# Performance work log

Hardware: AMD Instinct MI355X
Metric: run time of the kernel (lower is better)

Reference implementation:

```python
import jax, jax.numpy as jnp
import numpy as np

B, S, D = 2, 2048, 1024
H, DK, DV = 16, 64, 64
DF = 4096
EPS = 1e-5


def _layer_norm(x, g, b):
    mu = jnp.mean(x, axis=-1, keepdims=True)
    var = jnp.mean((x - mu) ** 2, axis=-1, keepdims=True)
    return (x - mu) * jax.lax.rsqrt(var + EPS) * g + b


def setup_inputs() -> dict:
    key = jax.random.key(0)
    ks = jax.random.split(key, 12)
    s = lambda fan_in: 1.0 / np.sqrt(fan_in)
    return {
        "enc_input": jax.random.normal(ks[0], (B, S, D), dtype=jnp.float32),
        "wq": jax.random.uniform(ks[1], (D, H * DK), jnp.float32, -s(D), s(D)),
        "wk": jax.random.uniform(ks[2], (D, H * DK), jnp.float32, -s(D), s(D)),
        "wv": jax.random.uniform(ks[3], (D, H * DV), jnp.float32, -s(D), s(D)),
        "wo": jax.random.uniform(ks[4], (H * DV, D), jnp.float32, -s(H * DV), s(H * DV)),
        "w1": jax.random.uniform(ks[5], (D, DF), jnp.float32, -s(D), s(D)),
        "b1": jax.random.uniform(ks[6], (DF,), jnp.float32, -s(D), s(D)),
        "w2": jax.random.uniform(ks[7], (DF, D), jnp.float32, -s(DF), s(DF)),
        "b2": jax.random.uniform(ks[8], (D,), jnp.float32, -s(DF), s(DF)),
        "ln1_g": jnp.ones((D,), jnp.float32),
        "ln1_b": jnp.zeros((D,), jnp.float32),
        "ln2_g": jnp.ones((D,), jnp.float32),
        "ln2_b": jnp.zeros((D,), jnp.float32),
    }


def reference(enc_input, wq, wk, wv, wo, w1, b1, w2, b2, ln1_g, ln1_b, ln2_g, ln2_b):
    x = enc_input
    # QKV projections -> [B, H, S, d]
    q = (x @ wq).reshape(B, S, H, DK).transpose(0, 2, 1, 3)
    k = (x @ wk).reshape(B, S, H, DK).transpose(0, 2, 1, 3)
    v = (x @ wv).reshape(B, S, H, DV).transpose(0, 2, 1, 3)
    # scaled dot-product attention (scale = 1/sqrt(d_k), dropout is identity at eval)
    score = jnp.einsum("bhqd,bhkd->bhqk", q, k) / jnp.sqrt(jnp.float32(DK))
    attn = jax.nn.softmax(score, axis=-1)
    ctx = jnp.einsum("bhqk,bhkd->bhqd", attn, v)
    ctx = ctx.transpose(0, 2, 1, 3).reshape(B, S, H * DV)
    atn_out = ctx @ wo
    # Add & Norm 1
    h = _layer_norm(x + atn_out, ln1_g, ln1_b)
    # FFN
    ffn = jax.nn.relu(h @ w1 + b1) @ w2 + b2
    # Add & Norm 2
    return _layer_norm(h + ffn, ln2_g, ln2_b)
```

## Files before the change

### kernel.cpp

```cpp
#include <hip/hip_runtime.h>
#include <hip/hip_bf16.h>

typedef __bf16 bf16;
typedef __bf16 bf16x4 __attribute__((ext_vector_type(4)));
typedef __bf16 bf16x8 __attribute__((ext_vector_type(8)));
typedef float  f32x4  __attribute__((ext_vector_type(4)));

#define KB 2
#define KS 2048
#define KD 1024
#define KH 16
#define KM (KB*KS)
#define KQKVN 3072
#define KDF 4096

__device__ __forceinline__ f32x4 mfma16(bf16x8 a, bf16x8 b, f32x4 c) {
  return __builtin_amdgcn_mfma_f32_16x16x32_bf16(a, b, c, 0, 0, 0);
}

__device__ __forceinline__ float exp2_hw(float x) {
  float r;
  asm("v_exp_f32 %0, %1" : "=v"(r) : "v"(x));
  return r;
}

__device__ __forceinline__ void g2l16(const bf16* g, bf16* l) {
  __builtin_amdgcn_global_load_lds(
      (const __attribute__((address_space(1))) unsigned int*)g,
      (__attribute__((address_space(3))) unsigned int*)l, 16, 0, 0);
}

__global__ __launch_bounds__(256) void cvt_bf16_kernel(const float* __restrict__ in,
                                                       bf16* __restrict__ out, int n) {
  int i = (blockIdx.x * 256 + threadIdx.x) * 4;
  if (i >= n) return;
  f32x4 v = *reinterpret_cast<const f32x4*>(in + i);
  bf16x4 o;
  o[0] = (bf16)v[0]; o[1] = (bf16)v[1]; o[2] = (bf16)v[2]; o[3] = (bf16)v[3];
  *reinterpret_cast<bf16x4*>(out + i) = o;
}

struct WT4 { const float* src[4]; bf16* dst[4]; };

__global__ __launch_bounds__(256) void wtrans4_kernel(WT4 jobs) {
  __shared__ float tile[32][33];
  const float* W = jobs.src[blockIdx.z];
  bf16* WT = jobs.dst[blockIdx.z];
  const int n0 = blockIdx.x * 32, k0 = blockIdx.y * 32;
  const int tx = threadIdx.x & 31, ty = threadIdx.x >> 5;
#pragma unroll
  for (int j = ty; j < 32; j += 8) tile[j][tx] = W[(size_t)(k0 + j) * 1024 + n0 + tx];
  __syncthreads();
#pragma unroll
  for (int j = ty; j < 32; j += 8)
    WT[(size_t)(n0 + j) * 1024 + k0 + tx] = (bf16)tile[tx][j];
}

__global__ __launch_bounds__(256) void wtrans_big_kernel(const float* __restrict__ w1,
                                                         bf16* __restrict__ w1T,
                                                         const float* __restrict__ w2,
                                                         bf16* __restrict__ w2T) {
  __shared__ float tile[32][33];
  const float* W; bf16* WT; int K, N, n0, k0;
  if (blockIdx.z == 0) {
    W = w1; WT = w1T; K = 1024; N = 4096;
    n0 = blockIdx.x * 32; k0 = blockIdx.y * 32;
  } else {
    W = w2; WT = w2T; K = 4096; N = 1024;
    n0 = blockIdx.y * 32; k0 = blockIdx.x * 32;
  }
  const int tx = threadIdx.x & 31, ty = threadIdx.x >> 5;
#pragma unroll
  for (int j = ty; j < 32; j += 8) tile[j][tx] = W[(size_t)(k0 + j) * N + n0 + tx];
  __syncthreads();
#pragma unroll
  for (int j = ty; j < 32; j += 8) WT[(size_t)(n0 + j) * K + k0 + tx] = (bf16)tile[tx][j];
}

struct P4 { bf16* p[4]; };

template <typename OUT_T, bool RELU, bool HAS_BIAS, bool SPLITK, bool QKVPACK>
__global__ __launch_bounds__(512, 2) void gemm8p(const bf16* __restrict__ A,
                                                 const bf16* __restrict__ BT,
                                                 OUT_T* __restrict__ C, P4 pr,
                                                 const float* __restrict__ bias,
                                                 int M, int N, int K, int Kslice) {
  extern __shared__ __align__(16) bf16 sm[];
  const int tid = threadIdx.x, lane = tid & 63, w = tid >> 6;
  const int wr = w >> 2, wc = w & 3;
  const int gx = gridDim.x;
  const int nwg = gx * gridDim.y;
  int flat = blockIdx.y * gx + blockIdx.x;
  flat = (flat & 7) * (nwg >> 3) + (flat >> 3);
  const int bn = (flat % gx) * 256;
  const int bm = (flat / gx) * 256;
  const int z = blockIdx.z;
  const int NT = (SPLITK ? Kslice : K) >> 6;
  const int lr = lane & 15, hi = lane >> 4;
  const int sqrow = tid >> 3;
  const int sslot = tid & 7;
  const bf16* Abase = A + (size_t)bm * K + (SPLITK ? z * Kslice : 0);
  const bf16* Bbase = BT + (size_t)bn * K + (SPLITK ? z * Kslice : 0);
  auto stageQ = [&](int t, int p) {
    const int row = p * 64 + sqrow;
    const int col = (sslot ^ (row & 7)) * 8;
    bf16* dst = sm + (size_t)(t & 1) * 32768 + p * 4096 + w * 512;
    g2l16(Abase + (size_t)row * K + t * 64 + col, dst);
    g2l16(Bbase + (size_t)row * K + t * 64 + col, dst + 16384);
  };
  f32x4 acc[8][4] = {};
  stageQ(0, 0); stageQ(0, 1); stageQ(0, 2); stageQ(0, 3);
  for (int t = 0; t < NT; t++) {
    const char* sa = (const char*)(sm + (size_t)(t & 1) * 32768);
    const char* sb = sa + 32768;
    if (t + 1 < NT) {
      stageQ(t + 1, 0);
      stageQ(t + 1, 1);
      asm volatile("s_waitcnt vmcnt(4)" ::: "memory");
    } else {
      asm volatile("s_waitcnt vmcnt(0)" ::: "memory");
    }
    __builtin_amdgcn_sched_barrier(0);
    __builtin_amdgcn_s_barrier();
    __builtin_amdgcn_sched_barrier(0);
    if (t + 1 < NT) { stageQ(t + 1, 2); stageQ(t + 1, 3); }
    bf16x8 af[4], bfr[4];
#pragma unroll
    for (int mfp = 0; mfp < 4; mfp++) {
      const int row = wr * 128 + mfp * 16 + lr;
      af[mfp] = *(const bf16x8*)(sa + row * 128 + ((hi ^ (row & 7)) * 16));
    }
#pragma unroll
    for (int nf = 0; nf < 4; nf++) {
      const int row = wc * 64 + nf * 16 + lr;
      bfr[nf] = *(const bf16x8*)(sb + row * 128 + ((hi ^ (row & 7)) * 16));
    }
    __builtin_amdgcn_s_setprio(1);
#pragma unroll
    for (int mfp = 0; mfp < 4; mfp++)
#pragma unroll
      for (int nf = 0; nf < 4; nf++)
        acc[mfp][nf] = mfma16(af[mfp], bfr[nf], acc[mfp][nf]);
    __builtin_amdgcn_s_setprio(0);
#pragma unroll
    for (int mfp = 0; mfp < 4; mfp++) {
      const int row = wr * 128 + 64 + mfp * 16 + lr;
      af[mfp] = *(const bf16x8*)(sa + row * 128 + ((hi ^ (row & 7)) * 16));
    }
    __builtin_amdgcn_s_setprio(1);
#pragma unroll
    for (int mfp = 0; mfp < 4; mfp++)
#pragma unroll
      for (int nf = 0; nf < 4; nf++)
        acc[4 + mfp][nf] = mfma16(af[mfp], bfr[nf], acc[4 + mfp][nf]);
    __builtin_amdgcn_s_setprio(0);
#pragma unroll
    for (int mfp = 0; mfp < 4; mfp++) {
      const int row = wr * 128 + mfp * 16 + lr;
      af[mfp] = *(const bf16x8*)(sa + row * 128 + (((4 + hi) ^ (row & 7)) * 16));
    }
#pragma unroll
    for (int nf = 0; nf < 4; nf++) {
      const int row = wc * 64 + nf * 16 + lr;
      bfr[nf] = *(const bf16x8*)(sb + row * 128 + (((4 + hi) ^ (row & 7)) * 16));
    }
    __builtin_amdgcn_s_setprio(1);
#pragma unroll
    for (int mfp = 0; mfp < 4; mfp++)
#pragma unroll
      for (int nf = 0; nf < 4; nf++)
        acc[mfp][nf] = mfma16(af[mfp], bfr[nf], acc[mfp][nf]);
    __builtin_amdgcn_s_setprio(0);
#pragma unroll
    for (int mfp = 0; mfp < 4; mfp++) {
      const int row = wr * 128 + 64 + mfp * 16 + lr;
      af[mfp] = *(const bf16x8*)(sa + row * 128 + (((4 + hi) ^ (row & 7)) * 16));
    }
    __builtin_amdgcn_s_setprio(1);
#pragma unroll
    for (int mfp = 0; mfp < 4; mfp++)
#pragma unroll
      for (int nf = 0; nf < 4; nf++)
        acc[4 + mfp][nf] = mfma16(af[mfp], bfr[nf], acc[4 + mfp][nf]);
    __builtin_amdgcn_s_setprio(0);
    __builtin_amdgcn_sched_barrier(0);
    __builtin_amdgcn_s_barrier();
    __builtin_amdgcn_sched_barrier(0);
  }
  const int rg = hi * 4, cl = lr;
  if (QKVPACK && (bn >> 10) == 1) {
    bf16* kp_ = pr.p[0];
    const int b_ = bm >> 11;
    const int sb_ = (bm & 2047) + wr * 128;
#pragma unroll
    for (int mf = 0; mf < 8; mf++)
#pragma unroll
      for (int nf = 0; nf < 4; nf++) {
        const int col_loc = (bn & 1023) + wc * 64 + nf * 16 + cl;
        const int hh = col_loc >> 6, dd = col_loc & 63;
        bf16* base = kp_ + (size_t)(b_ * 16 + hh) * (KS * 64) + dd;
#pragma unroll
        for (int i = 0; i < 4; i++)
          base[(size_t)(sb_ + mf * 16 + rg + i) * 64] = (bf16)acc[mf][nf][i];
      }
  } else if (QKVPACK && (bn >> 10) == 2) {
    bf16* vt_ = pr.p[1];
    const int b_ = bm >> 11;
    const int sb_ = (bm & 2047) + wr * 128;
    const int pib = ((hi & 2) << 3) | ((hi & 1) << 3);
#pragma unroll
    for (int mf = 0; mf < 8; mf++) {
      const int s_hi = sb_ + (mf >> 2) * 64;
      const int pibase = pib | ((mf & 2) << 4) | ((mf & 1) << 2);
#pragma unroll
      for (int nf = 0; nf < 4; nf++) {
        const int col_loc = (bn & 1023) + wc * 64 + nf * 16 + cl;
        const int hh = col_loc >> 6, dd = col_loc & 63;
        bf16x4 o;
#pragma unroll
        for (int i = 0; i < 4; i++) o[i] = (bf16)acc[mf][nf][i];
        *(bf16x4*)(vt_ + (size_t)(b_ * 16 + hh) * (64 * KS) +
                   (size_t)dd * KS + s_hi + pibase) = o;
      }
    }
  } else if (SPLITK) {
    bf16* P = pr.p[z];
#pragma unroll
    for (int mf = 0; mf < 8; mf++)
#pragma unroll
      for (int nf = 0; nf < 4; nf++) {
        const int col = bn + wc * 64 + nf * 16 + cl;
#pragma unroll
        for (int i = 0; i < 4; i++) {
          const int row = bm + wr * 128 + mf * 16 + rg + i;
          P[(size_t)row * N + col] = (bf16)acc[mf][nf][i];
        }
      }
  } else {
#pragma unroll
    for (int mf = 0; mf < 8; mf++)
#pragma unroll
      for (int nf = 0; nf < 4; nf++) {
        const int col = bn + wc * 64 + nf * 16 + cl;
        float bv = 0.f;
        if (HAS_BIAS) bv = bias[col];
#pragma unroll
        for (int i = 0; i < 4; i++) {
          const int row = bm + wr * 128 + mf * 16 + rg + i;
          float v = acc[mf][nf][i] + bv;
          if (RELU) v = fmaxf(v, 0.f);
          C[(size_t)row * N + col] = (OUT_T)v;
        }
      }
  }
}

template <typename OUT_T, bool RELU, bool HAS_BIAS, int BN>
__global__ __launch_bounds__(256) void gemm_bt(const bf16* __restrict__ A,
                                               const bf16* __restrict__ BT,
                                               OUT_T* __restrict__ C,
                                               const float* __restrict__ bias,
                                               int M, int N, int K) {
  constexpr int NF = BN / 32;
  __shared__ __align__(16) bf16 sa[2][128 * 32];
  __shared__ __align__(16) bf16 sb[2][BN * 32];
  const int t = threadIdx.x, lane = t & 63, w = t >> 6;
  const int gx = gridDim.x;
  const int nwg = gx * gridDim.y;
  int flat = blockIdx.y * gx + blockIdx.x;
  if ((nwg & 7) == 0) flat = (flat & 7) * (nwg >> 3) + (flat >> 3);
  const int bn = (flat % gx) * BN;
  const int bm = (flat / gx) * 128;
  const int wr = w >> 1, wc = w & 1;
  const int wcol = wc * (BN / 2);
  const int lr = lane & 15, lk = (lane >> 4) * 8;
  const int srow = w * 16 + (lane >> 2);
  const int scol = (lane & 3) * 8;
  f32x4 acc[4][NF] = {};
  const int NT = K >> 5;
  auto stage = [&](int kt, int buf) {
#pragma unroll
    for (int i = 0; i < 2; i++)
      g2l16(A + (size_t)(bm + i * 64 + srow) * K + kt * 32 + scol,
            &sa[buf][(i * 64 + w * 16) * 32]);
#pragma unroll
    for (int i = 0; i < BN / 64; i++)
      g2l16(BT + (size_t)(bn + i * 64 + srow) * K + kt * 32 + scol,
            &sb[buf][(i * 64 + w * 16) * 32]);
  };
  stage(0, 0);
  int cur = 0;
  for (int kt = 0; kt < NT; kt++) {
    __syncthreads();
    if (kt + 1 < NT) stage(kt + 1, cur ^ 1);
    bf16x8 af[4], bfr[NF];
#pragma unroll
    for (int m = 0; m < 4; m++)
      af[m] = *(const bf16x8*)&sa[cur][(wr * 64 + m * 16 + lr) * 32 + lk];
#pragma unroll
    for (int n = 0; n < NF; n++)
      bfr[n] = *(const bf16x8*)&sb[cur][(wcol + n * 16 + lr) * 32 + lk];
#pragma unroll
    for (int m = 0; m < 4; m++)
#pragma unroll
      for (int n = 0; n < NF; n++)
        acc[m][n] = mfma16(af[m], bfr[n], acc[m][n]);
    cur ^= 1;
  }
  const int rg = (lane >> 4) * 4, cl = lane & 15;
#pragma unroll
  for (int m = 0; m < 4; m++)
#pragma unroll
    for (int n = 0; n < NF; n++) {
      const int col = bn + wcol + n * 16 + cl;
      float bv = 0.f;
      if (HAS_BIAS) bv = bias[col];
#pragma unroll
      for (int i = 0; i < 4; i++) {
        const int row = bm + wr * 64 + m * 16 + rg + i;
        float v = acc[m][n][i] + bv;
        if (RELU) v = fmaxf(v, 0.f);
        C[(size_t)row * N + col] = (OUT_T)v;
      }
    }
}

__global__ __launch_bounds__(256) void attn_kernel(const bf16* __restrict__ qkv,
                                                   const bf16* __restrict__ kp,
                                                   const bf16* __restrict__ vt,
                                                   bf16* __restrict__ ctx) {
  __shared__ __align__(16) bf16 ksm[2][64 * 64];
  __shared__ __align__(16) bf16 vsm[2][64 * 64];
  const int t = threadIdx.x, lane = t & 63, w = t >> 6;
  const int flat = blockIdx.y * 32 + blockIdx.x;
  const int xcd = flat & 7, jj = flat >> 3;
  const int bh = xcd + 8 * (jj >> 5);
  const int qb = jj & 31;
  const int b = bh >> 4, h = bh & 15;
  const int qbase = qb * 64 + w * 16;
  const int lr = lane & 15, hi = lane >> 4;
  const int lk = hi * 8, rg = hi * 4, cl = lr;

  bf16x8 aq[2];
#pragma unroll
  for (int kk = 0; kk < 2; kk++) {
    bf16x8 v = *reinterpret_cast<const bf16x8*>(
        &qkv[(size_t)(b * KS + qbase + lr) * KQKVN + h * 64 + kk * 32 + lk]);
#pragma unroll
    for (int e = 0; e < 8; e++) v[e] = (bf16)((float)v[e] * 0.18033688f);
    aq[kk] = v;
  }
  bf16x8 ones;
#pragma unroll
  for (int j = 0; j < 8; j++) ones[j] = (bf16)1.0f;

  const bf16* kpb = kp + (size_t)bh * KS * 64;
  const bf16* vtb = vt + (size_t)bh * 64 * KS;

  auto stageKV = [&](int tt) {
    const int kt0 = tt * 64;
    bf16* kd = &ksm[tt & 1][0];
    bf16* vd = &vsm[tt & 1][0];
#pragma unroll
    for (int i = 0; i < 2; i++) {
      const int q = i * 4096 + w * 1024 + (lane << 4);
      const int row = q >> 7;
      const int slot = ((q >> 4) & 7) ^ (row & 7);
      g2l16(kpb + (size_t)(kt0 + row) * 64 + slot * 8, kd + ((i * 4096 + w * 1024) >> 1));
      g2l16(vtb + (size_t)row * KS + kt0 + slot * 8,   vd + ((i * 4096 + w * 1024) >> 1));
    }
  };

  f32x4 accd[4] = {};
  f32x4 lsumv = {};

  stageKV(0); stageKV(1);
  const int NT = KS / 64;
  for (int tt = 0; tt < NT; tt++) {
    if (tt + 1 < NT) asm volatile("s_waitcnt vmcnt(4)" ::: "memory");
    else             asm volatile("s_waitcnt vmcnt(0)" ::: "memory");
    __builtin_amdgcn_sched_barrier(0);
    __builtin_amdgcn_s_barrier();
    __builtin_amdgcn_sched_barrier(0);
    const char* kb = (const char*)&ksm[tt & 1][0];
    const char* vb = (const char*)&vsm[tt & 1][0];
    bf16x8 bk[4][2];
#pragma unroll
    for (int n = 0; n < 4; n++)
#pragma unroll
      for (int kk = 0; kk < 2; kk++) {
        const int row = n * 16 + lr;
        bk[n][kk] = *(const bf16x8*)(kb + row * 128 +
                                     ((kk * 64 + hi * 16) ^ ((row & 7) << 4)));
      }
    f32x4 sc[4] = {};
    __builtin_amdgcn_s_setprio(1);
#pragma unroll
    for (int n = 0; n < 4; n++)
#pragma unroll
      for (int kk = 0; kk < 2; kk++)
        sc[n] = mfma16(bk[n][kk], aq[kk], sc[n]);
    __builtin_amdgcn_s_setprio(0);
    bf16x8 pa[2];
    {
      float p[4][4];
#pragma unroll
      for (int n = 0; n < 4; n++)
#pragma unroll
        for (int i = 0; i < 4; i++)
          p[n][i] = exp2_hw(sc[n][i]);
#pragma unroll
      for (int kk = 0; kk < 2; kk++) {
        bf16x8 v;
#pragma unroll
        for (int j = 0; j < 8; j++) v[j] = (bf16)p[kk * 2 + (j >> 2)][j & 3];
        pa[kk] = v;
      }
    }
    bf16x8 bv[4][2];
#pragma unroll
    for (int dt = 0; dt < 4; dt++)
#pragma unroll
      for (int kk = 0; kk < 2; kk++) {
        const int row = dt * 16 + lr;
        bv[dt][kk] = *(const bf16x8*)(vb + row * 128 +
                                      ((kk * 64 + hi * 16) ^ ((row & 7) << 4)));
      }
    __builtin_amdgcn_s_setprio(1);
#pragma unroll
    for (int dt = 0; dt < 4; dt++)
#pragma unroll
      for (int kk = 0; kk < 2; kk++)
        accd[dt] = mfma16(pa[kk], bv[dt][kk], accd[dt]);
    lsumv = mfma16(pa[0], ones, lsumv);
    lsumv = mfma16(pa[1], ones, lsumv);
    __builtin_amdgcn_s_setprio(0);
    __builtin_amdgcn_sched_barrier(0);
    __builtin_amdgcn_s_barrier();
    __builtin_amdgcn_sched_barrier(0);
    if (tt + 2 < NT) stageKV(tt + 2);
  }
#pragma unroll
  for (int dt = 0; dt < 4; dt++)
#pragma unroll
    for (int i = 0; i < 4; i++)
      ctx[(size_t)(b * KS + qbase + rg + i) * KD + h * 64 + dt * 16 + cl] =
          (bf16)(accd[dt][i] / lsumv[i]);
}

template <bool ABF, bool BBF, bool OBF>
__global__ __launch_bounds__(256) void ln_kernel(const void* __restrict__ aptr,
                                                 const void* __restrict__ bptr,
                                                 const float* __restrict__ g,
                                                 const float* __restrict__ bet,
                                                 void* __restrict__ outp) {
  const int row = blockIdx.x;
  const int t = threadIdx.x;
  const int lane = t & 63, wid = t >> 6;
  float v[4];
  {
    float a[4], bb[4];
    if (ABF) {
      bf16x4 av = *reinterpret_cast<const bf16x4*>(
          (const bf16*)aptr + (size_t)row * KD + t * 4);
#pragma unroll
      for (int j = 0; j < 4; j++) a[j] = (float)av[j];
    } else {
      f32x4 av = *reinterpret_cast<const f32x4*>(
          (const float*)aptr + (size_t)row * KD + t * 4);
#pragma unroll
      for (int j = 0; j < 4; j++) a[j] = av[j];
    }
    if (BBF) {
      bf16x4 bv = *reinterpret_cast<const bf16x4*>(
          (const bf16*)bptr + (size_t)row * KD + t * 4);
#pragma unroll
      for (int j = 0; j < 4; j++) bb[j] = (float)bv[j];
    } else {
      f32x4 bv = *reinterpret_cast<const f32x4*>(
          (const float*)bptr + (size_t)row * KD + t * 4);
#pragma unroll
      for (int j = 0; j < 4; j++) bb[j] = bv[j];
    }
#pragma unroll
    for (int j = 0; j < 4; j++) v[j] = a[j] + bb[j];
  }
  float s = 0.f, s2 = 0.f;
#pragma unroll
  for (int j = 0; j < 4; j++) { s += v[j]; s2 += v[j] * v[j]; }
#pragma unroll
  for (int off = 32; off; off >>= 1) {
    s += __shfl_xor(s, off, 64);
    s2 += __shfl_xor(s2, off, 64);
  }
  __shared__ float red[8];
  if (lane == 0) { red[wid] = s; red[wid + 4] = s2; }
  __syncthreads();
  s = red[0] + red[1] + red[2] + red[3];
  s2 = red[4] + red[5] + red[6] + red[7];
  const float mu = s * (1.f / KD);
  const float var = s2 * (1.f / KD) - mu * mu;
  const float rs = rsqrtf(var + 1e-5f);
  if (OBF) {
    bf16x4 o;
#pragma unroll
    for (int j = 0; j < 4; j++)
      o[j] = (bf16)((v[j] - mu) * rs * g[t * 4 + j] + bet[t * 4 + j]);
    *reinterpret_cast<bf16x4*>((bf16*)outp + (size_t)row * KD + t * 4) = o;
  } else {
    f32x4 o;
#pragma unroll
    for (int j = 0; j < 4; j++)
      o[j] = (v[j] - mu) * rs * g[t * 4 + j] + bet[t * 4 + j];
    *reinterpret_cast<f32x4*>((float*)outp + (size_t)row * KD + t * 4) = o;
  }
}

__global__ __launch_bounds__(256) void ln2_fused_kernel(const bf16* __restrict__ hh,
                                                        const bf16* __restrict__ p0,
                                                        const bf16* __restrict__ p1,
                                                        const bf16* __restrict__ p2,
                                                        const bf16* __restrict__ p3,
                                                        const float* __restrict__ b2,
                                                        const float* __restrict__ g,
                                                        const float* __restrict__ bet,
                                                        float* __restrict__ outp) {
  const int row = blockIdx.x;
  const int t = threadIdx.x;
  const int lane = t & 63, wid = t >> 6;
  const size_t base = (size_t)row * KD + t * 4;
  bf16x4 hv = *(const bf16x4*)(hh + base);
  bf16x4 a0 = *(const bf16x4*)(p0 + base);
  bf16x4 a1 = *(const bf16x4*)(p1 + base);
  bf16x4 a2 = *(const bf16x4*)(p2 + base);
  bf16x4 a3 = *(const bf16x4*)(p3 + base);
  f32x4 bv = *(const f32x4*)(b2 + t * 4);
  float v[4];
#pragma unroll
  for (int j = 0; j < 4; j++)
    v[j] = (float)hv[j] + (float)a0[j] + (float)a1[j] + (float)a2[j] + (float)a3[j] + bv[j];
  float s = 0.f, s2 = 0.f;
#pragma unroll
  for (int j = 0; j < 4; j++) { s += v[j]; s2 += v[j] * v[j]; }
#pragma unroll
  for (int off = 32; off; off >>= 1) {
    s += __shfl_xor(s, off, 64);
    s2 += __shfl_xor(s2, off, 64);
  }
  __shared__ float red[8];
  if (lane == 0) { red[wid] = s; red[wid + 4] = s2; }
  __syncthreads();
  s = red[0] + red[1] + red[2] + red[3];
  s2 = red[4] + red[5] + red[6] + red[7];
  const float mu = s * (1.f / KD);
  const float var = s2 * (1.f / KD) - mu * mu;
  const float rs = rsqrtf(var + 1e-5f);
  f32x4 o;
#pragma unroll
  for (int j = 0; j < 4; j++)
    o[j] = (v[j] - mu) * rs * g[t * 4 + j] + bet[t * 4 + j];
  *reinterpret_cast<f32x4*>(outp + base) = o;
}

extern "C" void kernel_launch(void* const* d_in, const int* in_sizes, int n_in,
                              void* d_out, int out_size, void* d_ws, size_t ws_size,
                              hipStream_t stream) {
  const float* x     = (const float*)d_in[0];
  const float* wq    = (const float*)d_in[1];
  const float* wk    = (const float*)d_in[2];
  const float* wv    = (const float*)d_in[3];
  const float* wo    = (const float*)d_in[4];
  const float* w1    = (const float*)d_in[5];
  const float* b1    = (const float*)d_in[6];
  const float* w2    = (const float*)d_in[7];
  const float* b2    = (const float*)d_in[8];
  const float* ln1g  = (const float*)d_in[9];
  const float* ln1b  = (const float*)d_in[10];
  const float* ln2g  = (const float*)d_in[11];
  const float* ln2b  = (const float*)d_in[12];
  float* out = (float*)d_out;

  char* ws = (char*)d_ws;
  bf16*  x_bf   = (bf16*)(ws + 0);
  bf16*  wqkvT  = (bf16*)(ws + 8388608);
  bf16*  woT    = (bf16*)(ws + 14680064);
  bf16*  w1T    = (bf16*)(ws + 16777216);
  bf16*  w2T    = (bf16*)(ws + 25165824);
  bf16*  qkv    = (bf16*)(ws + 33554432);
  bf16*  kp     = (bf16*)(ws + 58720256);
  bf16*  vt     = (bf16*)(ws + 67108864);
  bf16*  ctx    = (bf16*)(ws + 75497472);
  bf16*  proj_bf= (bf16*)(ws + 83886080);
  bf16*  h_bf   = (bf16*)(ws + 8388608);
  bf16*  ffn1   = qkv;
  P4 pk;
  pk.p[0] = kp; pk.p[1] = vt; pk.p[2] = nullptr; pk.p[3] = nullptr;
  P4 pr;
  pr.p[0] = (bf16*)(ws + 0);
  pr.p[1] = (bf16*)(ws + 16777216);
  pr.p[2] = (bf16*)(ws + 67108864);
  pr.p[3] = (bf16*)(ws + 75497472);
  P4 pzero = {};

  cvt_bf16_kernel<<<dim3(KM * KD / 1024), 256, 0, stream>>>(x, x_bf, KM * KD);
  WT4 jobs;
  jobs.src[0] = wq; jobs.src[1] = wk; jobs.src[2] = wv; jobs.src[3] = wo;
  jobs.dst[0] = wqkvT;
  jobs.dst[1] = wqkvT + 1024 * 1024;
  jobs.dst[2] = wqkvT + 2048 * 1024;
  jobs.dst[3] = woT;
  wtrans4_kernel<<<dim3(32, 32, 4), 256, 0, stream>>>(jobs);
  wtrans_big_kernel<<<dim3(128, 32, 2), 256, 0, stream>>>(w1, w1T, w2, w2T);

  gemm8p<bf16, false, false, false, true>
      <<<dim3(KQKVN / 256, KM / 256, 1), 512, 131072, stream>>>(
      x_bf, wqkvT, qkv, pk, nullptr, KM, KQKVN, KD, KD);

  attn_kernel<<<dim3(KS / 64, KB * KH), 256, 0, stream>>>(qkv, kp, vt, ctx);

  gemm_bt<bf16, false, false, 64><<<dim3(KD / 64, KM / 128), 256, 0, stream>>>(
      ctx, woT, proj_bf, nullptr, KM, KD, KD);

  ln_kernel<true, true, true><<<dim3(KM), 256, 0, stream>>>(
      x_bf, proj_bf, ln1g, ln1b, h_bf);

  gemm8p<bf16, true, true, false, false>
      <<<dim3(KDF / 256, KM / 256, 1), 512, 131072, stream>>>(
      h_bf, w1T, ffn1, pzero, b1, KM, KDF, KD, KD);

  gemm8p<bf16, false, false, true, false>
      <<<dim3(KD / 256, KM / 256, 4), 512, 131072, stream>>>(
      ffn1, w2T, (bf16*)nullptr, pr, nullptr, KM, KD, KDF, KDF / 4);

  ln2_fused_kernel<<<dim3(KM), 256, 0, stream>>>(
      h_bf, pr.p[0], pr.p[1], pr.p[2], pr.p[3], b2, ln2g, ln2b, out);
}
```

Measured before the change: 221.6 us.

## Split attention over two KV halves with 32 queries per warp, add combine kernel

Each attention block now covers 128 queries (two 16-row query tiles per warp) but only half of the key/value sequence, so each staged K/V tile is reused across twice as many queries. The block writes unnormalized bf16 partial outputs and float row sums for its half. A new combine kernel adds the two halves and normalizes them into ctx. The cost is an extra launch, extra global traffic for the partials, more registers per warp, and bf16 rounding of unnormalized partial accumulators.

```diff
diff --git a/kernel.cpp b/kernel.cpp
--- a/kernel.cpp
+++ b/kernel.cpp
@@ -328,34 +328,42 @@
 __global__ __launch_bounds__(256) void attn_kernel(const bf16* __restrict__ qkv,
                                                    const bf16* __restrict__ kp,
                                                    const bf16* __restrict__ vt,
-                                                   bf16* __restrict__ ctx) {
+                                                   bf16* __restrict__ pa0,
+                                                   bf16* __restrict__ pa1,
+                                                   float* __restrict__ pl0,
+                                                   float* __restrict__ pl1) {
   __shared__ __align__(16) bf16 ksm[2][64 * 64];
   __shared__ __align__(16) bf16 vsm[2][64 * 64];
   const int t = threadIdx.x, lane = t & 63, w = t >> 6;
   const int flat = blockIdx.y * 32 + blockIdx.x;
   const int xcd = flat & 7, jj = flat >> 3;
   const int bh = xcd + 8 * (jj >> 5);
-  const int qb = jj & 31;
+  const int sub = jj & 31;
+  const int qb = sub >> 1, kv = sub & 1;
   const int b = bh >> 4, h = bh & 15;
-  const int qbase = qb * 64 + w * 16;
+  const int qbase = qb * 128 + w * 32;
   const int lr = lane & 15, hi = lane >> 4;
   const int lk = hi * 8, rg = hi * 4, cl = lr;
-
-  bf16x8 aq[2];
-#pragma unroll
-  for (int kk = 0; kk < 2; kk++) {
-    bf16x8 v = *reinterpret_cast<const bf16x8*>(
-        &qkv[(size_t)(b * KS + qbase + lr) * KQKVN + h * 64 + kk * 32 + lk]);
-#pragma unroll
-    for (int e = 0; e < 8; e++) v[e] = (bf16)((float)v[e] * 0.18033688f);
-    aq[kk] = v;
-  }
+  bf16* pac = kv ? pa1 : pa0;
+  float* pl = kv ? pl1 : pl0;
+
+  bf16x8 aq[2][2];
+#pragma unroll
+  for (int m = 0; m < 2; m++)
+#pragma unroll
+    for (int kk = 0; kk < 2; kk++) {
+      bf16x8 v = *reinterpret_cast<const bf16x8*>(
+          &qkv[(size_t)(b * KS + qbase + m * 16 + lr) * KQKVN + h * 64 + kk * 32 + lk]);
+#pragma unroll
+      for (int e = 0; e < 8; e++) v[e] = (bf16)((float)v[e] * 0.18033688f);
+      aq[m][kk] = v;
+    }
   bf16x8 ones;
 #pragma unroll
   for (int j = 0; j < 8; j++) ones[j] = (bf16)1.0f;
 
-  const bf16* kpb = kp + (size_t)bh * KS * 64;
-  const bf16* vtb = vt + (size_t)bh * 64 * KS;
+  const bf16* kpb = kp + (size_t)bh * KS * 64 + (size_t)(kv * 1024) * 64;
+  const bf16* vtb = vt + (size_t)bh * 64 * KS + kv * 1024;
 
   auto stageKV = [&](int tt) {
     const int kt0 = tt * 64;
@@ -371,11 +379,11 @@
     }
   };
 
-  f32x4 accd[4] = {};
-  f32x4 lsumv = {};
+  f32x4 accd[2][4] = {};
+  f32x4 lsumv[2] = {};
 
   stageKV(0); stageKV(1);
-  const int NT = KS / 64;
+  const int NT = KS / 64 / 2;
   for (int tt = 0; tt < NT; tt++) {
     if (tt + 1 < NT) asm volatile("s_waitcnt vmcnt(4)" ::: "memory");
     else             asm volatile("s_waitcnt vmcnt(0)" ::: "memory");
@@ -393,28 +401,31 @@
         bk[n][kk] = *(const bf16x8*)(kb + row * 128 +
                                      ((kk * 64 + hi * 16) ^ ((row & 7) << 4)));
       }
-    f32x4 sc[4] = {};
+    f32x4 sc[2][4] = {};
     __builtin_amdgcn_s_setprio(1);
 #pragma unroll
-    for (int n = 0; n < 4; n++)
-#pragma unroll
-      for (int kk = 0; kk < 2; kk++)
-        sc[n] = mfma16(bk[n][kk], aq[kk], sc[n]);
+    for (int m = 0; m < 2; m++)
+#pragma unroll
+      for (int n = 0; n < 4; n++)
+#pragma unroll
+        for (int kk = 0; kk < 2; kk++)
+          sc[m][n] = mfma16(bk[n][kk], aq[m][kk], sc[m][n]);
     __builtin_amdgcn_s_setprio(0);
-    bf16x8 pa[2];
-    {
+    bf16x8 pa[2][2];
+#pragma unroll
+    for (int m = 0; m < 2; m++) {
       float p[4][4];
 #pragma unroll
       for (int n = 0; n < 4; n++)
 #pragma unroll
         for (int i = 0; i < 4; i++)
-          p[n][i] = exp2_hw(sc[n][i]);
+          p[n][i] = exp2_hw(sc[m][n][i]);
 #pragma unroll
       for (int kk = 0; kk < 2; kk++) {
         bf16x8 v;
 #pragma unroll
         for (int j = 0; j < 8; j++) v[j] = (bf16)p[kk * 2 + (j >> 2)][j & 3];
-        pa[kk] = v;
+        pa[m][kk] = v;
       }
     }
     bf16x8 bv[4][2];
@@ -428,12 +439,15 @@
       }
     __builtin_amdgcn_s_setprio(1);
 #pragma unroll
-    for (int dt = 0; dt < 4; dt++)
-#pragma unroll
-      for (int kk = 0; kk < 2; kk++)
-        accd[dt] = mfma16(pa[kk], bv[dt][kk], accd[dt]);
-    lsumv = mfma16(pa[0], ones, lsumv);
-    lsumv = mfma16(pa[1], ones, lsumv);
+    for (int m = 0; m < 2; m++) {
+#pragma unroll
+      for (int dt = 0; dt < 4; dt++)
+#pragma unroll
+        for (int kk = 0; kk < 2; kk++)
+          accd[m][dt] = mfma16(pa[m][kk], bv[dt][kk], accd[m][dt]);
+      lsumv[m] = mfma16(pa[m][0], ones, lsumv[m]);
+      lsumv[m] = mfma16(pa[m][1], ones, lsumv[m]);
+    }
     __builtin_amdgcn_s_setprio(0);
     __builtin_amdgcn_sched_barrier(0);
     __builtin_amdgcn_s_barrier();
@@ -441,11 +455,34 @@
     if (tt + 2 < NT) stageKV(tt + 2);
   }
 #pragma unroll
-  for (int dt = 0; dt < 4; dt++)
-#pragma unroll
-    for (int i = 0; i < 4; i++)
-      ctx[(size_t)(b * KS + qbase + rg + i) * KD + h * 64 + dt * 16 + cl] =
-          (bf16)(accd[dt][i] / lsumv[i]);
+  for (int m = 0; m < 2; m++)
+#pragma unroll
+    for (int i = 0; i < 4; i++) {
+      const int row = b * KS + qbase + m * 16 + rg + i;
+      pl[(size_t)h * KM + row] = lsumv[m][i];
+#pragma unroll
+      for (int dt = 0; dt < 4; dt++)
+        pac[(size_t)row * KD + h * 64 + dt * 16 + cl] = (bf16)accd[m][dt][i];
+    }
+}
+
+__global__ __launch_bounds__(256) void attn_combine_kernel(const bf16* __restrict__ pa0,
+                                                           const bf16* __restrict__ pa1,
+                                                           const float* __restrict__ pl0,
+                                                           const float* __restrict__ pl1,
+                                                           bf16* __restrict__ ctx) {
+  const int r = blockIdx.x;
+  const int t = threadIdx.x;
+  const int h = t >> 4;
+  const size_t base = (size_t)r * KD + t * 4;
+  const float rl = 1.0f / (pl0[(size_t)h * KM + r] + pl1[(size_t)h * KM + r]);
+  bf16x4 a = *(const bf16x4*)(pa0 + base);
+  bf16x4 c = *(const bf16x4*)(pa1 + base);
+  bf16x4 o;
+#pragma unroll
+  for (int j = 0; j < 4; j++)
+    o[j] = (bf16)(((float)a[j] + (float)c[j]) * rl);
+  *(bf16x4*)(ctx + base) = o;
 }
 
 template <bool ABF, bool BBF, bool OBF>
@@ -589,8 +626,12 @@
   bf16*  qkv    = (bf16*)(ws + 33554432);
   bf16*  kp     = (bf16*)(ws + 58720256);
   bf16*  vt     = (bf16*)(ws + 67108864);
-  bf16*  ctx    = (bf16*)(ws + 75497472);
-  bf16*  proj_bf= (bf16*)(ws + 83886080);
+  bf16*  pacc0  = (bf16*)(ws + 75497472);
+  bf16*  pacc1  = (bf16*)(ws + 83886080);
+  float* pl0    = (float*)(ws + 8388608);
+  float* pl1    = (float*)(ws + 8388608 + 262144);
+  bf16*  ctx    = pacc0;
+  bf16*  proj_bf= pacc1;
   bf16*  h_bf   = (bf16*)(ws + 8388608);
   bf16*  ffn1   = qkv;
   P4 pk;
@@ -616,7 +657,9 @@
       <<<dim3(KQKVN / 256, KM / 256, 1), 512, 131072, stream>>>(
       x_bf, wqkvT, qkv, pk, nullptr, KM, KQKVN, KD, KD);
 
-  attn_kernel<<<dim3(KS / 64, KB * KH), 256, 0, stream>>>(qkv, kp, vt, ctx);
+  attn_kernel<<<dim3(32, 32), 256, 0, stream>>>(qkv, kp, vt, pacc0, pacc1, pl0, pl1);
+
+  attn_combine_kernel<<<dim3(KM), 256, 0, stream>>>(pacc0, pacc1, pl0, pl1, ctx);
 
   gemm_bt<bf16, false, false, 64><<<dim3(KD / 64, KM / 128), 256, 0, stream>>>(
       ctx, woT, proj_bf, nullptr, KM, KD, KD);
```

After: 225.9 us. About the same (+1.9%).
